# Kernel tuning notes

Hardware: AMD Instinct MI355X
Metric: run time of the kernel (lower is better)

The kernel has to match this reference:

```python
import jax, jax.numpy as jnp
import numpy as np

B, T, D_IN = 8, 1024, 320
L, H, DK, DV, DM, DI = 6, 8, 64, 64, 512, 2048


def _pe_table():
    pos = np.arange(T, dtype=np.float32)[:, None]
    div = np.exp(np.arange(0, DM, 2, dtype=np.float32) * (-np.log(10000.0) / DM))
    pe = np.zeros((T, DM), np.float32)
    pe[:, 0::2] = np.sin(pos * div)
    pe[:, 1::2] = np.cos(pos * div)
    return jnp.asarray(pe)


def setup_inputs() -> dict:
    key = jax.random.key(0)
    ks = jax.random.split(key, 16)
    rn = lambda k, shape, std: (jax.random.normal(k, shape, jnp.float32) * std)
    inp = {}
    inp["padded_input"] = jax.random.normal(ks[0], (B, T, D_IN), jnp.float32)
    inp["input_lengths"] = jax.random.randint(ks[1], (B,), T // 2, T + 1)
    # input projection + input layernorm (weights stored as [in, out])
    inp["w_in"] = rn(ks[2], (D_IN, DM), 0.02)
    inp["b_in"] = jnp.zeros((DM,), jnp.float32)
    inp["ln_in_g"] = jnp.ones((DM,), jnp.float32)
    inp["ln_in_b"] = jnp.zeros((DM,), jnp.float32)
    inp["pe"] = _pe_table()
    # stacked per-layer params, leading dim L
    inp["wq"] = rn(ks[3], (L, DM, H * DK), np.sqrt(2.0 / (DM + DK)))
    inp["bq"] = jnp.zeros((L, H * DK), jnp.float32)
    inp["wk"] = rn(ks[4], (L, DM, H * DK), np.sqrt(2.0 / (DM + DK)))
    inp["bk"] = jnp.zeros((L, H * DK), jnp.float32)
    inp["wv"] = rn(ks[5], (L, DM, H * DV), np.sqrt(2.0 / (DM + DV)))
    inp["bv"] = jnp.zeros((L, H * DV), jnp.float32)
    inp["wfc"] = rn(ks[6], (L, H * DV, DM), np.sqrt(2.0 / (H * DV + DM)))
    inp["bfc"] = jnp.zeros((L, DM), jnp.float32)
    inp["ln1_g"] = jnp.ones((L, DM), jnp.float32)
    inp["ln1_b"] = jnp.zeros((L, DM), jnp.float32)
    inp["w1"] = rn(ks[7], (L, DM, DI), np.sqrt(2.0 / (DM + DI)))
    inp["b1"] = jnp.zeros((L, DI), jnp.float32)
    inp["w2"] = rn(ks[8], (L, DI, DM), np.sqrt(2.0 / (DM + DI)))
    inp["b2"] = jnp.zeros((L, DM), jnp.float32)
    inp["ln2_g"] = jnp.ones((L, DM), jnp.float32)
    inp["ln2_b"] = jnp.zeros((L, DM), jnp.float32)
    return inp


def _layer_norm(x, g, b):
    mu = jnp.mean(x, axis=-1, keepdims=True)
    var = jnp.var(x, axis=-1, keepdims=True)
    return (x - mu) * jax.lax.rsqrt(var + 1e-5) * g + b


def _encoder(padded_input, input_lengths, w_in, b_in, ln_in_g, ln_in_b, pe,
             wq, bq, wk, bk, wv, bv, wfc, bfc, ln1_g, ln1_b,
             w1, b1, w2, b2, ln2_g, ln2_b):
    pos = jnp.arange(T)
    key_pad = pos[None, :] >= input_lengths[:, None]          # [B,T] True at pad
    non_pad = (~key_pad).astype(padded_input.dtype)[:, :, None]  # [B,T,1]
    scale = 1.0 / jnp.sqrt(jnp.float32(DK))

    x = _layer_norm(padded_input @ w_in + b_in, ln_in_g, ln_in_b) + pe[None]

    def body(x, p):
        Wq, Bq, Wk, Bk, Wv, Bv, Wfc, Bfc, G1, Bn1, W1, Bf1, W2, Bf2, G2, Bn2 = p
        res = x
        q = (x @ Wq + Bq).reshape(B, T, H, DK)
        k = (x @ Wk + Bk).reshape(B, T, H, DK)
        v = (x @ Wv + Bv).reshape(B, T, H, DV)
        attn = jnp.einsum('bqhd,bkhd->bhqk', q, k) * scale
        attn = jnp.where(key_pad[:, None, None, :], -jnp.inf, attn)
        attn = jax.nn.softmax(attn, axis=-1)
        o = jnp.einsum('bhqk,bkhd->bqhd', attn, v).reshape(B, T, H * DV)
        x = _layer_norm(o @ Wfc + Bfc + res, G1, Bn1) * non_pad
        res = x
        h = jax.nn.relu(x @ W1 + Bf1)
        x = _layer_norm(h @ W2 + Bf2 + res, G2, Bn2) * non_pad
        return x, None

    x, _ = jax.lax.scan(body, x, (wq, bq, wk, bk, wv, bv, wfc, bfc,
                                  ln1_g, ln1_b, w1, b1, w2, b2, ln2_g, ln2_b))
    return x


def reference(padded_input, input_lengths, w_in, b_in, ln_in_g, ln_in_b, pe,
              wq, bq, wk, bk, wv, bv, wfc, bfc, ln1_g, ln1_b,
              w1, b1, w2, b2, ln2_g, ln2_b):
    # dropout is identity in eval mode
    return _encoder(padded_input, input_lengths, w_in, b_in, ln_in_g, ln_in_b, pe,
                    wq, bq, wk, bk, wv, bv, wfc, bfc, ln1_g, ln1_b,
                    w1, b1, w2, b2, ln2_g, ln2_b)
```

## Files before the change

kernel.cpp:

```cpp
#include <hip/hip_runtime.h>
#include <hip/hip_bf16.h>


typedef unsigned short bh16;
typedef __bf16 bf16x8 __attribute__((ext_vector_type(8)));
typedef float f32x4 __attribute__((ext_vector_type(4)));
typedef unsigned int u32x4 __attribute__((ext_vector_type(4)));
typedef unsigned int u32x2 __attribute__((ext_vector_type(2)));

#define DEVI static __device__ __forceinline__

DEVI bh16 f2bf(float f) {
  union { float f; unsigned u; } x; x.f = f;
  unsigned r = x.u + 0x7fffu + ((x.u >> 16) & 1u);
  return (bh16)(r >> 16);
}
DEVI float bf2f(bh16 u) {
  union { unsigned u; float f; } x; x.u = ((unsigned)u) << 16; return x.f;
}
DEVI bf16x8 ld16(const bh16* p) {
  return __builtin_bit_cast(bf16x8, *(const u32x4*)p);
}
DEVI bf16x8 ld16b(const char* p) {
  return __builtin_bit_cast(bf16x8, *(const u32x4*)p);
}
DEVI f32x4 mfma16(bf16x8 a, bf16x8 b, f32x4 c) {
  return __builtin_amdgcn_mfma_f32_16x16x32_bf16(a, b, c, 0, 0, 0);
}
DEVI void async16(const void* g, void* l) {
  __builtin_amdgcn_global_load_lds(
      (const __attribute__((address_space(1))) void*)g,
      (__attribute__((address_space(3))) void*)l, 16, 0, 0);
}

__global__ __launch_bounds__(256) void tcvt(
    const float* __restrict__ in, bh16* __restrict__ out,
    int K, int N, long long inLS, long long outLS, int rowOff) {
  int l = blockIdx.z;
  in += (size_t)l * inLS;
  out += (size_t)l * outLS + (size_t)rowOff * K;
  __shared__ float t[32][33];
  int n0 = blockIdx.x * 32, k0 = blockIdx.y * 32;
  int tx = threadIdx.x & 31, ty = threadIdx.x >> 5;
#pragma unroll
  for (int i = 0; i < 4; i++)
    t[ty + 8 * i][tx] = in[(size_t)(k0 + ty + 8 * i) * N + n0 + tx];
  __syncthreads();
#pragma unroll
  for (int i = 0; i < 4; i++)
    out[(size_t)(n0 + ty + 8 * i) * K + k0 + tx] = f2bf(t[tx][ty + 8 * i]);
}

__global__ __launch_bounds__(256) void bcat(
    const float* __restrict__ bq, const float* __restrict__ bk,
    const float* __restrict__ bv, float* __restrict__ out) {
  int l = blockIdx.x;
  for (int j = threadIdx.x; j < 1536; j += 256) {
    float v = (j < 512) ? bq[l * 512 + j]
            : (j < 1024) ? bk[l * 512 + j - 512] : bv[l * 512 + j - 1024];
    out[l * 1536 + j] = v;
  }
}

__global__ __launch_bounds__(256) void cvt_in(
    const float* __restrict__ in, bh16* __restrict__ out, int n4) {
  int i = blockIdx.x * 256 + threadIdx.x;
  if (i < n4) {
    float4 v = ((const float4*)in)[i];
    u32x2 pk;
    pk[0] = (unsigned)f2bf(v.x) | ((unsigned)f2bf(v.y) << 16);
    pk[1] = (unsigned)f2bf(v.z) | ((unsigned)f2bf(v.w) << 16);
    *(u32x2*)(out + (size_t)i * 4) = pk;
  }
}

template <int BM, int BN, int RELU, int OUTF32, int QKV>
__global__ __launch_bounds__(256) void gemm_bt(
    const bh16* __restrict__ A, const bh16* __restrict__ Bt,
    const float* __restrict__ bias, void* __restrict__ Cout,
    bh16* __restrict__ vtOut, const int* __restrict__ lens,
    int M, int N, int K) {
  constexpr int BK = 64;
  __shared__ __align__(16) bh16 As[2][BM * BK];
  __shared__ __align__(16) bh16 Bs[2][BN * BK];
  const int tid = threadIdx.x;
  const int wave = tid >> 6, lane = tid & 63;
  const int lq = lane & 15, grp = lane >> 4;
  const int p = blockIdx.x;
  const int xcd = p & 7, idx = p >> 3;
  const int m0 = ((((idx & 7) << 3) | xcd)) * BM;
  const int n0 = (idx >> 3) * BN;
  if ((m0 & 1023) >= lens[m0 >> 10]) return;
  constexpr int FM = BM / 32, FN = BN / 32;
  const int wr = wave >> 1, wc = wave & 1;
  f32x4 acc[FM][FN] = {};

  const int nk = K / BK;
  auto stage = [&](int buf, int kt) {
#pragma unroll
    for (int i = 0; i < BM / 32; ++i) {
      int off = i * 4096 + wave * 1024 + lane * 16;
      int row = off >> 7, col = off & 127;
      int sw = (row & 7) << 4;
      const char* g =
          (const char*)A + ((size_t)(m0 + row) * K + kt * BK) * 2 + (col ^ sw);
      async16(g, (char*)As[buf] + off);
    }
#pragma unroll
    for (int i = 0; i < BN / 32; ++i) {
      int off = i * 4096 + wave * 1024 + lane * 16;
      int row = off >> 7, col = off & 127;
      int sw = (row & 7) << 4;
      const char* g =
          (const char*)Bt + ((size_t)(n0 + row) * K + kt * BK) * 2 + (col ^ sw);
      async16(g, (char*)Bs[buf] + off);
    }
  };

  stage(0, 0);
  for (int kt = 0; kt < nk; ++kt) {
    int cur = kt & 1;
    __syncthreads();
    if (kt + 1 < nk) stage(cur ^ 1, kt + 1);
#pragma unroll
    for (int kk = 0; kk < 2; ++kk) {
      bf16x8 af[FM], bfr[FN];
#pragma unroll
      for (int i = 0; i < FM; ++i) {
        int row = wr * (BM / 2) + i * 16 + lq;
        int sw = (row & 7) << 4;
        af[i] = ld16b((char*)As[cur] + row * 128 + ((kk * 64 + grp * 16) ^ sw));
      }
#pragma unroll
      for (int j = 0; j < FN; ++j) {
        int row = wc * (BN / 2) + j * 16 + lq;
        int sw = (row & 7) << 4;
        bfr[j] = ld16b((char*)Bs[cur] + row * 128 + ((kk * 64 + grp * 16) ^ sw));
      }
      __builtin_amdgcn_s_setprio(1);
#pragma unroll
      for (int i = 0; i < FM; ++i)
#pragma unroll
        for (int j = 0; j < FN; ++j)
          acc[i][j] = mfma16(af[i], bfr[j], acc[i][j]);
      __builtin_amdgcn_s_setprio(0);
    }
  }
  if (QKV && n0 >= 1024) {
#pragma unroll
    for (int i = 0; i < FM; ++i) {
#pragma unroll
      for (int j = 0; j < FN; ++j) {
        int col = n0 + wc * (BN / 2) + j * 16 + lq;
        float bv = bias[col];
        int vc = col - 1024;
        int t0 = m0 + wr * (BM / 2) + i * 16 + grp * 4;
        int bb = t0 >> 10, tl = t0 & 1023;
        u32x2 pk;
        pk[0] = (unsigned)f2bf(acc[i][j][0] + bv) |
                ((unsigned)f2bf(acc[i][j][1] + bv) << 16);
        pk[1] = (unsigned)f2bf(acc[i][j][2] + bv) |
                ((unsigned)f2bf(acc[i][j][3] + bv) << 16);
        *(u32x2*)&vtOut[((size_t)(bb * 512 + vc)) * 1024 + tl] = pk;
      }
    }
    return;
  }
#pragma unroll
  for (int i = 0; i < FM; ++i) {
#pragma unroll
    for (int j = 0; j < FN; ++j) {
      int col = n0 + wc * (BN / 2) + j * 16 + lq;
      float bv = bias[col];
#pragma unroll
      for (int r = 0; r < 4; ++r) {
        int row = m0 + wr * (BM / 2) + i * 16 + grp * 4 + r;
        float v = acc[i][j][r] + bv;
        if (RELU) v = fmaxf(v, 0.f);
        if (OUTF32) ((float*)Cout)[(size_t)row * N + col] = v;
        else ((bh16*)Cout)[(size_t)row * N + col] = f2bf(v);
      }
    }
  }
}

__global__ __launch_bounds__(256) void ln_pe_k(
    const float* __restrict__ in, const float* __restrict__ g,
    const float* __restrict__ bta, const float* __restrict__ pe,
    bh16* __restrict__ xb) {
  int wave = threadIdx.x >> 6, lane = threadIdx.x & 63;
  int row = blockIdx.x * 4 + wave;
  int t = row & 1023;
  const float* xr = in + (size_t)row * 512 + lane * 8;
  float4 a0 = ((const float4*)xr)[0], a1 = ((const float4*)xr)[1];
  float v[8] = {a0.x, a0.y, a0.z, a0.w, a1.x, a1.y, a1.z, a1.w};
  float s = 0.f, ss = 0.f;
#pragma unroll
  for (int j = 0; j < 8; j++) { s += v[j]; ss += v[j] * v[j]; }
#pragma unroll
  for (int m = 1; m < 64; m <<= 1) { s += __shfl_xor(s, m); ss += __shfl_xor(ss, m); }
  float mu = s * (1.f / 512.f);
  float rstd = rsqrtf(ss * (1.f / 512.f) - mu * mu + 1e-5f);
  int c0 = lane * 8;
  float o[8];
  u32x4 pk;
#pragma unroll
  for (int j = 0; j < 8; j++) {
    int c = c0 + j;
    o[j] = (v[j] - mu) * rstd * g[c] + bta[c] + pe[(size_t)t * 512 + c];
  }
#pragma unroll
  for (int j = 0; j < 4; j++)
    pk[j] = (unsigned)f2bf(o[2 * j]) | ((unsigned)f2bf(o[2 * j + 1]) << 16);
  *(u32x4*)(xb + (size_t)row * 512 + c0) = pk;
}

__global__ __launch_bounds__(256) void ln_res_k(
    const bh16* __restrict__ gout, const bh16* res,
    const float* __restrict__ g, const float* __restrict__ bta,
    const int* __restrict__ lens, bh16* xb, float* fout) {
  int wave = threadIdx.x >> 6, lane = threadIdx.x & 63;
  int row = blockIdx.x * 4 + wave;
  int b = row >> 10, t = row & 1023;
  float nonpad = (t < lens[b]) ? 1.f : 0.f;
  int c0 = lane * 8;
  u32x4 graw = *(const u32x4*)(gout + (size_t)row * 512 + c0);
  u32x4 rraw = *(const u32x4*)(res + (size_t)row * 512 + c0);
  float v[8];
#pragma unroll
  for (int j = 0; j < 4; j++) {
    v[2 * j] = bf2f((bh16)(graw[j] & 0xffffu)) + bf2f((bh16)(rraw[j] & 0xffffu));
    v[2 * j + 1] = bf2f((bh16)(graw[j] >> 16)) + bf2f((bh16)(rraw[j] >> 16));
  }
  float s = 0.f, ss = 0.f;
#pragma unroll
  for (int j = 0; j < 8; j++) { s += v[j]; ss += v[j] * v[j]; }
#pragma unroll
  for (int m = 1; m < 64; m <<= 1) { s += __shfl_xor(s, m); ss += __shfl_xor(ss, m); }
  float mu = s * (1.f / 512.f);
  float rstd = rsqrtf(ss * (1.f / 512.f) - mu * mu + 1e-5f);
  float o[8];
  u32x4 pk;
#pragma unroll
  for (int j = 0; j < 8; j++) {
    int c = c0 + j;
    o[j] = ((v[j] - mu) * rstd * g[c] + bta[c]) * nonpad;
  }
#pragma unroll
  for (int j = 0; j < 4; j++)
    pk[j] = (unsigned)f2bf(o[2 * j]) | ((unsigned)f2bf(o[2 * j + 1]) << 16);
  *(u32x4*)(xb + (size_t)row * 512 + c0) = pk;
  if (fout) {
    float4* xo = (float4*)(fout + (size_t)row * 512 + c0);
    xo[0] = make_float4(o[0], o[1], o[2], o[3]);
    xo[1] = make_float4(o[4], o[5], o[6], o[7]);
  }
}

__global__ __launch_bounds__(512) void attn_k(
    const bh16* __restrict__ qkv, const bh16* __restrict__ vt,
    const int* __restrict__ lens, bh16* __restrict__ o) {
  constexpr int LDP = 72;
  __shared__ __align__(16) char Ks[2][8192];
  __shared__ __align__(16) char Vs[2][8192];
  __shared__ __align__(16) bh16 P[8][16 * LDP];
  int p = blockIdx.x;
  int xcd = p & 7, s = p >> 3;
  int bh = ((s & 7) << 3) | xcd;
  int qt = s >> 3;
  int b = bh >> 3, h = bh & 7;
  int len = lens[b];
  if (qt * 128 >= len) return;
  int tid = threadIdx.x;
  int wave = tid >> 6, lane = tid & 63;
  int lq = lane & 15, grp = lane >> 4;

  size_t qrow = (size_t)(b * 1024 + qt * 128 + wave * 16 + lq);
  const bh16* Qp = qkv + qrow * 1536 + h * 64;
  bf16x8 qf0 = ld16(Qp + grp * 8);
  bf16x8 qf1 = ld16(Qp + 32 + grp * 8);
  const char* Kbase = (const char*)(qkv + (size_t)(b * 1024) * 1536 + 512 + h * 64);
  const char* Vbase = (const char*)(vt + (size_t)(bh * 64) * 1024);
  bh16* Pw = P[wave];

  f32x4 oacc[4] = {};
  float m = -1e30f, lsum = 0.f;
  int nkb = (len + 63) >> 6;

  auto stage = [&](int buf, int kb) {
    int off = tid * 16;
    int row = off >> 7, cb = off & 127;
    int sw = (row & 7) << 4;
    async16(Kbase + (size_t)(kb * 64 + row) * 3072 + (cb ^ sw), Ks[buf] + off);
    async16(Vbase + (size_t)row * 2048 + kb * 128 + (cb ^ sw), Vs[buf] + off);
  };

  stage(0, 0);
  for (int kb = 0; kb < nkb; ++kb) {
    int cur = kb & 1;
    __syncthreads();
    if (kb + 1 < nkb) stage(cur ^ 1, kb + 1);
    int k64 = kb * 64;
    f32x4 st[4];
    __builtin_amdgcn_s_setprio(1);
#pragma unroll
    for (int sv = 0; sv < 4; ++sv) {
      int row = sv * 16 + lq, sw = (row & 7) << 4;
      const char* kp = Ks[cur] + row * 128;
      f32x4 z = {};
      z = mfma16(ld16b(kp + ((grp * 16) ^ sw)), qf0, z);
      z = mfma16(ld16b(kp + ((64 + grp * 16) ^ sw)), qf1, z);
      st[sv] = z;
    }
    __builtin_amdgcn_s_setprio(0);
    float tmax = -1e30f;
    if (k64 + 64 > len) {
#pragma unroll
      for (int sv = 0; sv < 4; ++sv)
#pragma unroll
        for (int r = 0; r < 4; ++r) {
          int key = k64 + sv * 16 + grp * 4 + r;
          float v = st[sv][r] * 0.125f;
          v = (key < len) ? v : -1e30f;
          st[sv][r] = v;
          tmax = fmaxf(tmax, v);
        }
    } else {
#pragma unroll
      for (int sv = 0; sv < 4; ++sv)
#pragma unroll
        for (int r = 0; r < 4; ++r) {
          float v = st[sv][r] * 0.125f;
          st[sv][r] = v;
          tmax = fmaxf(tmax, v);
        }
    }
    tmax = fmaxf(tmax, __shfl_xor(tmax, 16));
    tmax = fmaxf(tmax, __shfl_xor(tmax, 32));
    float newm = fmaxf(m, tmax);
    if (!__all(newm - m <= 8.f)) {
      float sc = __expf(m - newm);
      m = newm;
      lsum *= sc;
#pragma unroll
      for (int r = 0; r < 4; ++r) {
        float scr = __shfl(sc, grp * 4 + r);
#pragma unroll
        for (int dt = 0; dt < 4; ++dt) oacc[dt][r] *= scr;
      }
    }
    float rs = 0.f;
#pragma unroll
    for (int sv = 0; sv < 4; ++sv) {
      float p0 = __expf(st[sv][0] - m), p1 = __expf(st[sv][1] - m);
      float p2 = __expf(st[sv][2] - m), p3 = __expf(st[sv][3] - m);
      rs += (p0 + p1) + (p2 + p3);
      u32x2 pk;
      pk[0] = (unsigned)f2bf(p0) | ((unsigned)f2bf(p1) << 16);
      pk[1] = (unsigned)f2bf(p2) | ((unsigned)f2bf(p3) << 16);
      *(u32x2*)&Pw[lq * LDP + sv * 16 + grp * 4] = pk;
    }
    rs += __shfl_xor(rs, 16);
    rs += __shfl_xor(rs, 32);
    lsum += rs;
#pragma unroll
    for (int kk = 0; kk < 2; ++kk) {
      bf16x8 pa = ld16(Pw + lq * LDP + kk * 32 + grp * 8);
      __builtin_amdgcn_s_setprio(1);
#pragma unroll
      for (int dt = 0; dt < 4; ++dt) {
        int row = dt * 16 + lq, sw = (row & 7) << 4;
        bf16x8 vfr = ld16b(Vs[cur] + row * 128 + ((kk * 64 + grp * 16) ^ sw));
        oacc[dt] = mfma16(pa, vfr, oacc[dt]);
      }
      __builtin_amdgcn_s_setprio(0);
    }
  }
#pragma unroll
  for (int r = 0; r < 4; ++r) {
    float li = __shfl(lsum, grp * 4 + r);
    float inv = 1.f / li;
    int row = qt * 128 + wave * 16 + grp * 4 + r;
    bh16* orow = o + (size_t)(b * 1024 + row) * 512 + h * 64;
#pragma unroll
    for (int dt = 0; dt < 4; ++dt) orow[dt * 16 + lq] = f2bf(oacc[dt][r] * inv);
  }
}

extern "C" void kernel_launch(void* const* d_in, const int* in_sizes, int n_in,
                              void* d_out, int out_size, void* d_ws, size_t ws_size,
                              hipStream_t stream) {
  const float* padded = (const float*)d_in[0];
  const int* lens = (const int*)d_in[1];
  const float* w_in = (const float*)d_in[2];
  const float* b_in = (const float*)d_in[3];
  const float* ln_in_g = (const float*)d_in[4];
  const float* ln_in_b = (const float*)d_in[5];
  const float* pe = (const float*)d_in[6];
  const float* wq = (const float*)d_in[7];
  const float* bq = (const float*)d_in[8];
  const float* wk = (const float*)d_in[9];
  const float* bk = (const float*)d_in[10];
  const float* wv = (const float*)d_in[11];
  const float* bv = (const float*)d_in[12];
  const float* wfc = (const float*)d_in[13];
  const float* bfc = (const float*)d_in[14];
  const float* ln1_g = (const float*)d_in[15];
  const float* ln1_b = (const float*)d_in[16];
  const float* w1 = (const float*)d_in[17];
  const float* b1 = (const float*)d_in[18];
  const float* w2 = (const float*)d_in[19];
  const float* b2 = (const float*)d_in[20];
  const float* ln2_g = (const float*)d_in[21];
  const float* ln2_b = (const float*)d_in[22];

  char* ws = (char*)d_ws;
  size_t off = 0;
  auto alloc = [&](size_t bytes) -> char* {
    char* p = ws + off;
    off += (bytes + 255) & ~(size_t)255;
    return p;
  };
  bh16* WinT  = (bh16*)alloc((size_t)512 * 320 * 2);
  bh16* WqkvT = (bh16*)alloc((size_t)6 * 1536 * 512 * 2);
  bh16* WfcT  = (bh16*)alloc((size_t)6 * 512 * 512 * 2);
  bh16* W1T   = (bh16*)alloc((size_t)6 * 2048 * 512 * 2);
  bh16* W2T   = (bh16*)alloc((size_t)6 * 512 * 2048 * 2);
  float* bqkv = (float*)alloc((size_t)6 * 1536 * 4);
  bh16* xb    = (bh16*)alloc((size_t)8192 * 512 * 2);
  bh16* qkvb  = (bh16*)alloc((size_t)8192 * 1536 * 2);
  bh16* vt    = (bh16*)alloc((size_t)64 * 64 * 1024 * 2);
  bh16* ob    = (bh16*)alloc((size_t)8192 * 512 * 2);
  float* tmp32 = (float*)alloc((size_t)8192 * 512 * 4);
  bh16* tmp16 = (bh16*)alloc((size_t)8192 * 512 * 2);
  bh16* hbuf  = (bh16*)alloc((size_t)8192 * 2048 * 2);
  bh16* padb  = hbuf;
  if (off > ws_size) return;

  tcvt<<<dim3(16, 10, 1), 256, 0, stream>>>(w_in, WinT, 320, 512, 0, 0, 0);
  tcvt<<<dim3(16, 16, 6), 256, 0, stream>>>(wq, WqkvT, 512, 512, 512 * 512, 1536 * 512, 0);
  tcvt<<<dim3(16, 16, 6), 256, 0, stream>>>(wk, WqkvT, 512, 512, 512 * 512, 1536 * 512, 512);
  tcvt<<<dim3(16, 16, 6), 256, 0, stream>>>(wv, WqkvT, 512, 512, 512 * 512, 1536 * 512, 1024);
  tcvt<<<dim3(16, 16, 6), 256, 0, stream>>>(wfc, WfcT, 512, 512, 512 * 512, 512 * 512, 0);
  tcvt<<<dim3(64, 16, 6), 256, 0, stream>>>(w1, W1T, 512, 2048, (long long)512 * 2048, (long long)2048 * 512, 0);
  tcvt<<<dim3(16, 64, 6), 256, 0, stream>>>(w2, W2T, 2048, 512, (long long)2048 * 512, (long long)512 * 2048, 0);
  bcat<<<6, 256, 0, stream>>>(bq, bk, bv, bqkv);
  cvt_in<<<2560, 256, 0, stream>>>(padded, padb, 655360);

  gemm_bt<128, 64, 0, 1, 0><<<512, 256, 0, stream>>>(
      padb, WinT, b_in, tmp32, nullptr, lens, 8192, 512, 320);
  ln_pe_k<<<2048, 256, 0, stream>>>(tmp32, ln_in_g, ln_in_b, pe, xb);

  for (int l = 0; l < 6; ++l) {
    gemm_bt<128, 128, 0, 0, 1><<<768, 256, 0, stream>>>(
        xb, WqkvT + (size_t)l * 1536 * 512, bqkv + l * 1536, qkvb, vt, lens,
        8192, 1536, 512);
    attn_k<<<512, 512, 0, stream>>>(qkvb, vt, lens, ob);
    gemm_bt<128, 64, 0, 0, 0><<<512, 256, 0, stream>>>(
        ob, WfcT + (size_t)l * 512 * 512, bfc + l * 512, tmp16, nullptr, lens,
        8192, 512, 512);
    ln_res_k<<<2048, 256, 0, stream>>>(tmp16, xb, ln1_g + l * 512, ln1_b + l * 512,
                                       lens, xb, nullptr);
    gemm_bt<128, 128, 1, 0, 0><<<1024, 256, 0, stream>>>(
        xb, W1T + (size_t)l * 2048 * 512, b1 + l * 2048, hbuf, nullptr, lens,
        8192, 2048, 512);
    gemm_bt<128, 64, 0, 0, 0><<<512, 256, 0, stream>>>(
        hbuf, W2T + (size_t)l * 512 * 2048, b2 + l * 512, tmp16, nullptr, lens,
        8192, 512, 2048);
    ln_res_k<<<2048, 256, 0, stream>>>(tmp16, xb, ln2_g + l * 512, ln2_b + l * 512,
                                       lens, xb, (l == 5) ? (float*)d_out : nullptr);
  }
}
```

Before: 823.0 us.

## Merge weight transpose launches and shrink GEMM M-tiles for more blocks

The seven weight-transpose/convert launches become one flat-grid kernel that decodes which weight and tile each block handles, removing per-launch overhead. The Wfc, W1 and W2 GEMMs switch from 128-row to 64-row M tiles and double their grid sizes. The block-index to tile mapping is generalized so it works with either tile height, and early exit on padded rows is preserved. This is meant to give more blocks per CU and finer skipping of padded rows, at the cost of less reuse of B tiles per block.

```diff
diff --git a/kernel.cpp b/kernel.cpp
--- a/kernel.cpp
+++ b/kernel.cpp
@@ -33,14 +33,8 @@
       (__attribute__((address_space(3))) void*)l, 16, 0, 0);
 }
 
-__global__ __launch_bounds__(256) void tcvt(
-    const float* __restrict__ in, bh16* __restrict__ out,
-    int K, int N, long long inLS, long long outLS, int rowOff) {
-  int l = blockIdx.z;
-  in += (size_t)l * inLS;
-  out += (size_t)l * outLS + (size_t)rowOff * K;
+DEVI void tcvt_body(const float* in, bh16* out, int K, int N, int n0, int k0) {
   __shared__ float t[32][33];
-  int n0 = blockIdx.x * 32, k0 = blockIdx.y * 32;
   int tx = threadIdx.x & 31, ty = threadIdx.x >> 5;
 #pragma unroll
   for (int i = 0; i < 4; i++)
@@ -49,6 +43,49 @@
 #pragma unroll
   for (int i = 0; i < 4; i++)
     out[(size_t)(n0 + ty + 8 * i) * K + k0 + tx] = f2bf(t[tx][ty + 8 * i]);
+}
+
+__global__ __launch_bounds__(256) void tcvt_all(
+    const float* __restrict__ w_in, const float* __restrict__ wq,
+    const float* __restrict__ wk, const float* __restrict__ wv,
+    const float* __restrict__ wfc, const float* __restrict__ w1,
+    const float* __restrict__ w2, bh16* __restrict__ WinT,
+    bh16* __restrict__ WqkvT, bh16* __restrict__ WfcT,
+    bh16* __restrict__ W1T, bh16* __restrict__ W2T) {
+  int p = blockIdx.x;
+  const float* in; bh16* out; int K, N, rem;
+  if (p < 160) {
+    in = w_in; out = WinT; K = 320; N = 512; rem = p;
+  } else if (p < 160 + 1536) {
+    rem = p - 160; int l = rem >> 8; rem &= 255;
+    in = wq + (size_t)l * 512 * 512; out = WqkvT + (size_t)l * 1536 * 512;
+    K = 512; N = 512;
+  } else if (p < 160 + 3072) {
+    rem = p - 160 - 1536; int l = rem >> 8; rem &= 255;
+    in = wk + (size_t)l * 512 * 512;
+    out = WqkvT + (size_t)l * 1536 * 512 + (size_t)512 * 512;
+    K = 512; N = 512;
+  } else if (p < 160 + 4608) {
+    rem = p - 160 - 3072; int l = rem >> 8; rem &= 255;
+    in = wv + (size_t)l * 512 * 512;
+    out = WqkvT + (size_t)l * 1536 * 512 + (size_t)1024 * 512;
+    K = 512; N = 512;
+  } else if (p < 160 + 6144) {
+    rem = p - 160 - 4608; int l = rem >> 8; rem &= 255;
+    in = wfc + (size_t)l * 512 * 512; out = WfcT + (size_t)l * 512 * 512;
+    K = 512; N = 512;
+  } else if (p < 160 + 6144 + 6144) {
+    rem = p - 160 - 6144; int l = rem >> 10; rem &= 1023;
+    in = w1 + (size_t)l * 512 * 2048; out = W1T + (size_t)l * 2048 * 512;
+    K = 512; N = 2048;
+  } else {
+    rem = p - 160 - 12288; int l = rem >> 10; rem &= 1023;
+    in = w2 + (size_t)l * 2048 * 512; out = W2T + (size_t)l * 512 * 2048;
+    K = 2048; N = 512;
+  }
+  int nt = N >> 5;
+  int n0 = (rem % nt) * 32, k0 = (rem / nt) * 32;
+  tcvt_body(in, out, K, N, n0, k0);
 }
 
 __global__ __launch_bounds__(256) void bcat(
@@ -81,6 +118,8 @@
     bh16* __restrict__ vtOut, const int* __restrict__ lens,
     int M, int N, int K) {
   constexpr int BK = 64;
+  constexpr int PX = (8192 / BM) / 8;
+  constexpr int PXS = (PX == 8) ? 3 : 4;
   __shared__ __align__(16) bh16 As[2][BM * BK];
   __shared__ __align__(16) bh16 Bs[2][BN * BK];
   const int tid = threadIdx.x;
@@ -88,8 +127,8 @@
   const int lq = lane & 15, grp = lane >> 4;
   const int p = blockIdx.x;
   const int xcd = p & 7, idx = p >> 3;
-  const int m0 = ((((idx & 7) << 3) | xcd)) * BM;
-  const int n0 = (idx >> 3) * BN;
+  const int m0 = (((idx & (PX - 1)) << 3) | xcd) * BM;
+  const int n0 = (idx >> PXS) * BN;
   if ((m0 & 1023) >= lens[m0 >> 10]) return;
   constexpr int FM = BM / 32, FN = BN / 32;
   const int wr = wave >> 1, wc = wave & 1;
@@ -437,13 +476,8 @@
   bh16* padb  = hbuf;
   if (off > ws_size) return;
 
-  tcvt<<<dim3(16, 10, 1), 256, 0, stream>>>(w_in, WinT, 320, 512, 0, 0, 0);
-  tcvt<<<dim3(16, 16, 6), 256, 0, stream>>>(wq, WqkvT, 512, 512, 512 * 512, 1536 * 512, 0);
-  tcvt<<<dim3(16, 16, 6), 256, 0, stream>>>(wk, WqkvT, 512, 512, 512 * 512, 1536 * 512, 512);
-  tcvt<<<dim3(16, 16, 6), 256, 0, stream>>>(wv, WqkvT, 512, 512, 512 * 512, 1536 * 512, 1024);
-  tcvt<<<dim3(16, 16, 6), 256, 0, stream>>>(wfc, WfcT, 512, 512, 512 * 512, 512 * 512, 0);
-  tcvt<<<dim3(64, 16, 6), 256, 0, stream>>>(w1, W1T, 512, 2048, (long long)512 * 2048, (long long)2048 * 512, 0);
-  tcvt<<<dim3(16, 64, 6), 256, 0, stream>>>(w2, W2T, 2048, 512, (long long)2048 * 512, (long long)512 * 2048, 0);
+  tcvt_all<<<18592, 256, 0, stream>>>(w_in, wq, wk, wv, wfc, w1, w2,
+                                      WinT, WqkvT, WfcT, W1T, W2T);
   bcat<<<6, 256, 0, stream>>>(bq, bk, bv, bqkv);
   cvt_in<<<2560, 256, 0, stream>>>(padded, padb, 655360);
 
@@ -456,15 +490,15 @@
         xb, WqkvT + (size_t)l * 1536 * 512, bqkv + l * 1536, qkvb, vt, lens,
         8192, 1536, 512);
     attn_k<<<512, 512, 0, stream>>>(qkvb, vt, lens, ob);
-    gemm_bt<128, 64, 0, 0, 0><<<512, 256, 0, stream>>>(
+    gemm_bt<64, 64, 0, 0, 0><<<1024, 256, 0, stream>>>(
         ob, WfcT + (size_t)l * 512 * 512, bfc + l * 512, tmp16, nullptr, lens,
         8192, 512, 512);
     ln_res_k<<<2048, 256, 0, stream>>>(tmp16, xb, ln1_g + l * 512, ln1_b + l * 512,
                                        lens, xb, nullptr);
-    gemm_bt<128, 128, 1, 0, 0><<<1024, 256, 0, stream>>>(
+    gemm_bt<64, 128, 1, 0, 0><<<2048, 256, 0, stream>>>(
         xb, W1T + (size_t)l * 2048 * 512, b1 + l * 2048, hbuf, nullptr, lens,
         8192, 2048, 512);
-    gemm_bt<128, 64, 0, 0, 0><<<512, 256, 0, stream>>>(
+    gemm_bt<64, 64, 0, 0, 0><<<1024, 256, 0, stream>>>(
         hbuf, W2T + (size_t)l * 512 * 2048, b2 + l * 512, tmp16, nullptr, lens,
         8192, 512, 2048);
     ln_res_k<<<2048, 256, 0, stream>>>(tmp16, xb, ln2_g + l * 512, ln2_b + l * 512,
```

After: 803.1 us. 1.02x faster.
